# Kernel optimization log

Measured on AMD Instinct MI355X. Metric: run time of the kernel, lower is better.

Reference implementation:

```python
import jax, jax.numpy as jnp
import numpy as np

N_NODES = 50000
N_EDGES = 800000
IN_DIM = 128
HID = 64
OUT_DIM = 128
N_GRAPHS = 128


def setup_inputs() -> dict:
    key = jax.random.key(0)
    ks = jax.random.split(key, 16)

    def lin(k, fan_in, fan_out):
        k1, k2 = jax.random.split(k)
        bound = 1.0 / np.sqrt(fan_in)
        W = jax.random.uniform(k1, (fan_in, fan_out), jnp.float32, -bound, bound)
        b = jax.random.uniform(k2, (fan_out,), jnp.float32, -bound, bound)
        return W, b

    x = jax.random.normal(ks[0], (N_NODES, IN_DIM), jnp.float32)
    edge_index = jax.random.randint(ks[1], (2, N_EDGES), 0, N_NODES, jnp.int64)
    batch = jnp.sort(jax.random.randint(ks[2], (N_NODES,), 0, N_GRAPHS, jnp.int64))

    W_in, b_in = lin(ks[3], IN_DIM, HID)
    W1_0, b1_0 = lin(ks[4], HID, HID)
    W2_0, b2_0 = lin(ks[5], HID, HID)
    W1_1, b1_1 = lin(ks[6], HID, HID)
    W2_1, b2_1 = lin(ks[7], HID, HID)
    W_out, b_out = lin(ks[8], HID, OUT_DIM)

    return dict(x=x, edge_index=edge_index, batch=batch,
                W_in=W_in, b_in=b_in,
                W1_0=W1_0, b1_0=b1_0, W2_0=W2_0, b2_0=b2_0,
                W1_1=W1_1, b1_1=b1_1, W2_1=W2_1, b2_1=b2_1,
                W_out=W_out, b_out=b_out)


def _gin_conv(x, src, dst, W1, b1, W2, b2):
    # aggr[i] = sum_{(s,i) in E} x[s]; GIN (eps=0): h = MLP(x + aggr)
    msgs = x[src]  # [E, HID] gather
    aggr = jax.ops.segment_sum(msgs, dst, num_segments=N_NODES)
    h = x + aggr
    h = jax.nn.relu(h @ W1 + b1)
    return h @ W2 + b2


def reference(x, edge_index, batch,
              W_in, b_in,
              W1_0, b1_0, W2_0, b2_0,
              W1_1, b1_1, W2_1, b2_1,
              W_out, b_out):
    src, dst = edge_index[0], edge_index[1]
    h = x @ W_in + b_in  # proj_in
    # conv 0 (+ReLU; dropout is identity in eval mode)
    h = jax.nn.relu(_gin_conv(h, src, dst, W1_0, b1_0, W2_0, b2_0))
    # conv 1
    h = jax.nn.relu(_gin_conv(h, src, dst, W1_1, b1_1, W2_1, b2_1))
    h = h @ W_out + b_out  # proj_out -> [N, OUT_DIM]
    # global mean pool over graphs
    sums = jax.ops.segment_sum(h, batch, num_segments=N_GRAPHS)
    counts = jax.ops.segment_sum(jnp.ones((h.shape[0],), h.dtype), batch, num_segments=N_GRAPHS)
    graph_emb = sums / jnp.maximum(counts, 1.0)[:, None]  # [N_GRAPHS, OUT_DIM]
    return graph_emb
```

## Files before the change

### kernel.cpp

```cpp
#include <hip/hip_runtime.h>
#include <hip/hip_fp16.h>

#define N_NODES   50000
#define N_EDGES   800000
#define IN_DIM    128
#define HID       64
#define OUT_DIM   128
#define N_GRAPHS  128

#define NBKT      196
#define BBLK      392
#define BSTRIDE   5120
#define CAP       40

#define OFF_GCUR   0
#define OFF_GSUM   196
#define OFF_GSTART 8388
#define OFF_ROWPTR 8518
#define OFF_SRCL   58520
#define OFF_EPAIRS 458520
#define OFF_HA     1462040
#define OFF_HB     2262040

typedef float v2f __attribute__((ext_vector_type(2)));

__device__ __forceinline__ void acc_fp8x8(float acc[8], const uint2 w) {
    const v2f a = __builtin_amdgcn_cvt_pk_f32_fp8(w.x, false);
    const v2f b = __builtin_amdgcn_cvt_pk_f32_fp8(w.x, true);
    const v2f c = __builtin_amdgcn_cvt_pk_f32_fp8(w.y, false);
    const v2f d = __builtin_amdgcn_cvt_pk_f32_fp8(w.y, true);
    acc[0] += a.x; acc[1] += a.y; acc[2] += b.x; acc[3] += b.y;
    acc[4] += c.x; acc[5] += c.y; acc[6] += d.x; acc[7] += d.y;
}

__device__ __forceinline__ uint2 pack_fp8x8(const float f[8]) {
    int w0 = 0, w1 = 0;
    w0 = __builtin_amdgcn_cvt_pk_fp8_f32(f[0], f[1], w0, false);
    w0 = __builtin_amdgcn_cvt_pk_fp8_f32(f[2], f[3], w0, true);
    w1 = __builtin_amdgcn_cvt_pk_fp8_f32(f[4], f[5], w1, false);
    w1 = __builtin_amdgcn_cvt_pk_fp8_f32(f[6], f[7], w1, true);
    uint2 r; r.x = (unsigned)w0; r.y = (unsigned)w1;
    return r;
}

#define BG_SMEM_BYTES 32144

__device__ __forceinline__ void role_bucket(char* smem, const int* __restrict__ ei,
                                            int* __restrict__ gcur,
                                            unsigned int* __restrict__ epairs,
                                            int bid) {
    int* lcnt = (int*)smem;
    unsigned int* stage = (unsigned int*)(smem + NBKT * 4);
    const int t = threadIdx.x;
    for (int i = t; i < NBKT; i += 256) lcnt[i] = 0;
    __syncthreads();
    for (int e0 = bid * 512; e0 < N_EDGES; e0 += BBLK * 512) {
#pragma unroll
        for (int half = 0; half < 2; ++half) {
            const int e = e0 + half * 256 + t;
            if (e < N_EDGES) {
                const unsigned int src = (unsigned int)ei[e];
                const unsigned int dst = (unsigned int)ei[N_EDGES + e];
                const int b = dst >> 8;
                const unsigned int pk = src | (dst << 16);
                const int pos = atomicAdd(&lcnt[b], 1);
                if (pos < CAP) stage[b * CAP + pos] = pk;
                else {
                    const int gp = atomicAdd(&gcur[b], 1);
                    epairs[b * BSTRIDE + gp] = pk;
                }
            }
        }
        __syncthreads();
        if (t < NBKT) {
            int n = lcnt[t]; if (n > CAP) n = CAP;
            if (n >= 16) {
                const int f = n & ~15;
                const int base = atomicAdd(&gcur[t], f);
                if ((base & 3) == 0) {
                    for (int i = 0; i < f; i += 4)
                        *(uint4*)&epairs[t * BSTRIDE + base + i] =
                            *(const uint4*)&stage[t * CAP + i];
                } else {
                    for (int i = 0; i < f; ++i)
                        epairs[t * BSTRIDE + base + i] = stage[t * CAP + i];
                }
                for (int i = 0; i < n - f; ++i)
                    stage[t * CAP + i] = stage[t * CAP + f + i];
                lcnt[t] = n - f;
            } else {
                lcnt[t] = n;
            }
        }
        __syncthreads();
    }
    if (t < NBKT) {
        const int n = lcnt[t];
        if (n > 0) {
            const int base = atomicAdd(&gcur[t], n);
            for (int i = 0; i < n; ++i)
                epairs[t * BSTRIDE + base + i] = stage[t * CAP + i];
        }
    }
}

__device__ __forceinline__ void role_gbound(const int* __restrict__ batch,
                                            int* __restrict__ gstart, int bid) {
    const int n = bid * 256 + threadIdx.x;
    if (n >= N_NODES) return;
    const int b = batch[n];
    if (n == 0) {
        for (int g = 0; g <= b; ++g) gstart[g] = 0;
    } else {
        const int p = batch[n - 1];
        for (int g = p + 1; g <= b; ++g) gstart[g] = n;
    }
    if (n == N_NODES - 1) {
        for (int g = b + 1; g <= N_GRAPHS; ++g) gstart[g] = N_NODES;
    }
}

__global__ __launch_bounds__(256) void k_bg(
        const int* __restrict__ ei, const int* __restrict__ batch,
        int* __restrict__ gcur, unsigned int* __restrict__ epairs,
        int* __restrict__ gstart) {
    __shared__ __attribute__((aligned(16))) char smem[BG_SMEM_BYTES];
    const int bid = blockIdx.x;
    if (bid < BBLK) role_bucket(smem, ei, gcur, epairs, bid);
    else            role_gbound(batch, gstart, bid - BBLK);
}

#define S_X2 132
#define CP_SMEM_BYTES 33280

__device__ __forceinline__ void role_csr(char* smem, const int* __restrict__ gcur,
                                         const unsigned int* __restrict__ epairs,
                                         int* __restrict__ rowptr,
                                         unsigned short* __restrict__ srclist, int b) {
    int* lhist = (int*)smem;
    int* lcur  = lhist + 256;
    int* pws   = lcur + 256;
    int* wtot  = pws + 4;
    int* lsrc  = wtot + 4;
    const int t = threadIdx.x;
    const int lane = t & 63, wv = t >> 6;

    int po = 0;
    for (int j = t; j < b; j += 256) po += gcur[j];
#pragma unroll
    for (int m = 32; m; m >>= 1) po += __shfl_xor(po, m, 64);
    if (lane == 0) pws[wv] = po;
    lhist[t] = 0;
    __syncthreads();
    const int base = pws[0] + pws[1] + pws[2] + pws[3];
    const int cnt = gcur[b];

    for (int i = t; i < cnt; i += 256)
        atomicAdd(&lhist[(epairs[b * BSTRIDE + i] >> 16) & 255], 1);
    __syncthreads();

    const int d = lhist[t];
    int incl = d;
#pragma unroll
    for (int off = 1; off < 64; off <<= 1) {
        const int u = __shfl_up(incl, off, 64);
        if (lane >= off) incl += u;
    }
    if (lane == 63) wtot[wv] = incl;
    __syncthreads();
    int woff = 0;
#pragma unroll
    for (int i = 0; i < 4; ++i) woff += (i < wv) ? wtot[i] : 0;
    const int excl = woff + incl - d;
    lcur[t] = excl;
    const int node = b * 256 + t;
    if (node < N_NODES) rowptr[node] = base + excl;
    if (b == NBKT - 1 && t == 0) rowptr[N_NODES] = base + cnt;
    __syncthreads();

    for (int i = t; i < cnt; i += 256) {
        const unsigned int u = epairs[b * BSTRIDE + i];
        const int pos = atomicAdd(&lcur[(u >> 16) & 255], 1);
        lsrc[pos] = (int)(u & 0xFFFFu);
    }
    __syncthreads();
    for (int i = t; i < cnt; i += 256)
        srclist[base + i] = (unsigned short)lsrc[i];
}

__device__ __forceinline__ void role_proj(char* smem, const float* __restrict__ x,
                                          const float* __restrict__ W,
                                          const float* __restrict__ b,
                                          unsigned char* __restrict__ h8, int bid) {
    __half* A = (__half*)smem;
    float* Wl = (float*)(smem + 64 * S_X2 * 2);
    const int t = threadIdx.x;
    const int nb = bid * 64;
    for (int i = t; i < 64 * HID; i += 256) Wl[i] = W[i];
    for (int i = t; i < 64 * (IN_DIM / 4); i += 256) {
        const int n = i >> 5;
        const int k4 = (i & 31) * 4;
        float4 val = make_float4(0.f, 0.f, 0.f, 0.f);
        if (nb + n < N_NODES)
            val = *(const float4*)(x + (size_t)(nb + n) * IN_DIM + k4);
        union { uint2 u; __half2 h[2]; } pk;
        pk.h[0] = __floats2half2_rn(val.x, val.y);
        pk.h[1] = __floats2half2_rn(val.z, val.w);
        *(uint2*)&A[n * S_X2 + k4] = pk.u;
    }
    __syncthreads();

    const int ln = t & 31;
    const int c0 = (t >> 5) * 8;
    float acc[2][8];
#pragma unroll
    for (int j = 0; j < 2; ++j)
#pragma unroll
        for (int c = 0; c < 8; ++c) acc[j][c] = b[c0 + c];
    for (int k = 0; k < 64; ++k) {
        const float a0 = __half2float(A[ln * S_X2 + k]);
        const float a1 = __half2float(A[(ln + 32) * S_X2 + k]);
        const float4 wA = *(const float4*)&Wl[k * HID + c0];
        const float4 wB = *(const float4*)&Wl[k * HID + c0 + 4];
        const float w[8] = {wA.x, wA.y, wA.z, wA.w, wB.x, wB.y, wB.z, wB.w};
#pragma unroll
        for (int c = 0; c < 8; ++c) {
            acc[0][c] = fmaf(a0, w[c], acc[0][c]);
            acc[1][c] = fmaf(a1, w[c], acc[1][c]);
        }
    }
    __syncthreads();
    for (int i = t; i < 64 * HID; i += 256) Wl[i] = W[64 * HID + i];
    __syncthreads();
    for (int k = 64; k < 128; ++k) {
        const float a0 = __half2float(A[ln * S_X2 + k]);
        const float a1 = __half2float(A[(ln + 32) * S_X2 + k]);
        const float4 wA = *(const float4*)&Wl[(k - 64) * HID + c0];
        const float4 wB = *(const float4*)&Wl[(k - 64) * HID + c0 + 4];
        const float w[8] = {wA.x, wA.y, wA.z, wA.w, wB.x, wB.y, wB.z, wB.w};
#pragma unroll
        for (int c = 0; c < 8; ++c) {
            acc[0][c] = fmaf(a0, w[c], acc[0][c]);
            acc[1][c] = fmaf(a1, w[c], acc[1][c]);
        }
    }
#pragma unroll
    for (int j = 0; j < 2; ++j) {
        const int n = nb + ln + 32 * j;
        if (n < N_NODES) {
            const uint2 p = pack_fp8x8(acc[j]);
            *(uint2*)(h8 + (size_t)n * HID + c0) = p;
        }
    }
}

__global__ __launch_bounds__(256) void k_cp(
        const int* __restrict__ gcur, const unsigned int* __restrict__ epairs,
        const float* __restrict__ x, const float* __restrict__ W,
        const float* __restrict__ b,
        int* __restrict__ rowptr, unsigned short* __restrict__ srcl,
        unsigned char* __restrict__ h8) {
    __shared__ __attribute__((aligned(16))) char smem[CP_SMEM_BYTES];
    const int bid = blockIdx.x;
    if (bid < NBKT) role_csr(smem, gcur, epairs, rowptr, srcl, bid);
    else            role_proj(smem, x, W, b, h8, bid - NBKT);
}

#define S_A 65
template<int POOL>
__global__ __launch_bounds__(256, 4) void k_conv_t(
        const unsigned char* __restrict__ hin8,
        const int* __restrict__ rowptr, const unsigned short* __restrict__ srclist,
        const float* __restrict__ W1, const float* __restrict__ b1,
        const float* __restrict__ W2, const float* __restrict__ b2,
        unsigned char* __restrict__ hout8,
        const int* __restrict__ batch, float* __restrict__ gsum) {
    __shared__ float A[64 * S_A];
    __shared__ float Wl[HID * HID];
    const int t = threadIdx.x;
    for (int i = t; i < HID * HID; i += 256) Wl[i] = W1[i];

    const int nb = blockIdx.x * 64;
    const int grp = t >> 3;
    const int q = t & 7;
#pragma unroll
    for (int pass = 0; pass < 2; ++pass) {
        const int nloc = pass * 32 + grp;
        const int node = nb + nloc;
        float acc[8] = {0.f, 0.f, 0.f, 0.f, 0.f, 0.f, 0.f, 0.f};
        if (node < N_NODES) {
            acc_fp8x8(acc, *(const uint2*)(hin8 + (size_t)node * HID + q * 8));
            const int beg = rowptr[node];
            const int end = rowptr[node + 1];
            int e = beg;
            for (; e + 8 <= end; e += 8) {
                int s[8];
#pragma unroll
                for (int i = 0; i < 8; ++i) s[i] = srclist[e + i];
                uint2 r[8];
#pragma unroll
                for (int i = 0; i < 8; ++i)
                    r[i] = *(const uint2*)(hin8 + (size_t)s[i] * HID + q * 8);
#pragma unroll
                for (int i = 0; i < 8; ++i) acc_fp8x8(acc, r[i]);
            }
            for (; e < end; ++e)
                acc_fp8x8(acc, *(const uint2*)(hin8 + (size_t)srclist[e] * HID + q * 8));
        }
        float* dst = &A[nloc * S_A + q * 8];
#pragma unroll
        for (int i = 0; i < 8; ++i) dst[i] = acc[i];
    }
    __syncthreads();

    const int ln = t & 31;
    const int c0 = (t >> 5) * 8;
    float bb[8];
#pragma unroll
    for (int c = 0; c < 8; ++c) bb[c] = b1[c0 + c];

    float acc2[2][8];
#pragma unroll
    for (int j = 0; j < 2; ++j)
#pragma unroll
        for (int c = 0; c < 8; ++c) acc2[j][c] = bb[c];
    for (int k = 0; k < HID; ++k) {
        const float a0 = A[ln * S_A + k];
        const float a1 = A[(ln + 32) * S_A + k];
        const float4 wA = *(const float4*)&Wl[k * HID + c0];
        const float4 wB = *(const float4*)&Wl[k * HID + c0 + 4];
        const float w[8] = {wA.x, wA.y, wA.z, wA.w, wB.x, wB.y, wB.z, wB.w};
#pragma unroll
        for (int c = 0; c < 8; ++c) {
            acc2[0][c] = fmaf(a0, w[c], acc2[0][c]);
            acc2[1][c] = fmaf(a1, w[c], acc2[1][c]);
        }
    }
    __syncthreads();
#pragma unroll
    for (int j = 0; j < 2; ++j) {
        float* dst = &A[(ln + 32 * j) * S_A + c0];
#pragma unroll
        for (int c = 0; c < 8; ++c) dst[c] = fmaxf(acc2[j][c], 0.0f);
    }
    for (int i = t; i < HID * HID; i += 256) Wl[i] = W2[i];
#pragma unroll
    for (int c = 0; c < 8; ++c) bb[c] = b2[c0 + c];
    __syncthreads();

#pragma unroll
    for (int j = 0; j < 2; ++j)
#pragma unroll
        for (int c = 0; c < 8; ++c) acc2[j][c] = bb[c];
    for (int k = 0; k < HID; ++k) {
        const float a0 = A[ln * S_A + k];
        const float a1 = A[(ln + 32) * S_A + k];
        const float4 wA = *(const float4*)&Wl[k * HID + c0];
        const float4 wB = *(const float4*)&Wl[k * HID + c0 + 4];
        const float w[8] = {wA.x, wA.y, wA.z, wA.w, wB.x, wB.y, wB.z, wB.w};
#pragma unroll
        for (int c = 0; c < 8; ++c) {
            acc2[0][c] = fmaf(a0, w[c], acc2[0][c]);
            acc2[1][c] = fmaf(a1, w[c], acc2[1][c]);
        }
    }
    if constexpr (POOL) {
        const int nlast = (nb + 64 <= N_NODES) ? nb + 63 : N_NODES - 1;
        const int g0 = batch[nb];
        const int g1 = batch[nlast];
        int myg[2];
#pragma unroll
        for (int j = 0; j < 2; ++j) {
            const int n = nb + ln + 32 * j;
            myg[j] = (n < N_NODES) ? batch[n] : -1;
        }
        for (int g = g0; g <= g1; ++g) {
#pragma unroll
            for (int j = 0; j < 2; ++j) {
#pragma unroll
                for (int c = 0; c < 8; ++c) {
                    float v = (myg[j] == g) ? fmaxf(acc2[j][c], 0.0f) : 0.0f;
#pragma unroll
                    for (int m = 16; m; m >>= 1) v += __shfl_xor(v, m, 64);
                    if (ln == 0) atomicAdd(&gsum[g * HID + c0 + c], v);
                }
            }
        }
    } else {
#pragma unroll
        for (int j = 0; j < 2; ++j) {
            const int n = nb + ln + 32 * j;
            if (n < N_NODES) {
                float f[8];
#pragma unroll
                for (int c = 0; c < 8; ++c) f[c] = fmaxf(acc2[j][c], 0.0f);
                const uint2 p = pack_fp8x8(f);
                *(uint2*)(hout8 + (size_t)n * HID + c0) = p;
            }
        }
    }
}

__global__ __launch_bounds__(128) void k_out(
        const float* __restrict__ gsum, const int* __restrict__ gstart,
        const float* __restrict__ Wo, const float* __restrict__ bo,
        float* __restrict__ out) {
    __shared__ float mean[HID];
    const int g = blockIdx.x;
    const int t = threadIdx.x;
    const int cnt = gstart[g + 1] - gstart[g];
    if (t < HID)
        mean[t] = (cnt > 0) ? gsum[g * HID + t] / (float)cnt : 0.0f;
    __syncthreads();
    float o = 0.0f;
    for (int k = 0; k < HID; ++k)
        o = fmaf(mean[k], Wo[k * OUT_DIM + t], o);
    out[g * OUT_DIM + t] = (cnt > 0) ? o + bo[t] : 0.0f;
}

extern "C" void kernel_launch(void* const* d_in, const int* in_sizes, int n_in,
                              void* d_out, int out_size, void* d_ws, size_t ws_size,
                              hipStream_t stream) {
    const float* x     = (const float*)d_in[0];
    const int*   ei    = (const int*)d_in[1];
    const int*   batch = (const int*)d_in[2];
    const float* W_in  = (const float*)d_in[3];
    const float* b_in  = (const float*)d_in[4];
    const float* W1_0  = (const float*)d_in[5];
    const float* b1_0  = (const float*)d_in[6];
    const float* W2_0  = (const float*)d_in[7];
    const float* b2_0  = (const float*)d_in[8];
    const float* W1_1  = (const float*)d_in[9];
    const float* b1_1  = (const float*)d_in[10];
    const float* W2_1  = (const float*)d_in[11];
    const float* b2_1  = (const float*)d_in[12];
    const float* W_out = (const float*)d_in[13];
    const float* b_out = (const float*)d_in[14];
    float* out = (float*)d_out;

    unsigned int*   wsw    = (unsigned int*)d_ws;
    int*            gcur   = (int*)(wsw + OFF_GCUR);
    float*          gsum   = (float*)(wsw + OFF_GSUM);
    int*            gstart = (int*)(wsw + OFF_GSTART);
    int*            rowptr = (int*)(wsw + OFF_ROWPTR);
    unsigned short* srcl   = (unsigned short*)(wsw + OFF_SRCL);
    unsigned int*   epairs = (unsigned int*)(wsw + OFF_EPAIRS);
    unsigned char*  hA     = (unsigned char*)(wsw + OFF_HA);
    unsigned char*  hB     = (unsigned char*)(wsw + OFF_HB);

    const int pi_blocks = (N_NODES + 63) / 64;
    const int cv_blocks = (N_NODES + 63) / 64;
    const int bg_blocks = BBLK + NBKT;
    const int cp_blocks = NBKT + pi_blocks;

    hipMemsetAsync(gcur, 0, (NBKT + N_GRAPHS * HID) * sizeof(int), stream);
    k_bg<<<bg_blocks, 256, 0, stream>>>(ei, batch, gcur, epairs, gstart);
    k_cp<<<cp_blocks, 256, 0, stream>>>(gcur, epairs, x, W_in, b_in,
                                        rowptr, srcl, hA);
    k_conv_t<0><<<cv_blocks, 256, 0, stream>>>(hA, rowptr, srcl,
                                               W1_0, b1_0, W2_0, b2_0, hB,
                                               batch, gsum);
    k_conv_t<1><<<cv_blocks, 256, 0, stream>>>(hB, rowptr, srcl,
                                               W1_1, b1_1, W2_1, b2_1, hA,
                                               batch, gsum);
    k_out<<<N_GRAPHS, 128, 0, stream>>>(gsum, gstart, W_out, b_out, out);
}
```

Baseline: 204.8 us.

## Use bf16 MFMA for input projection and GIN MLP layers

Replaces the scalar FP32 FMA loops in the input projection and both GIN MLPs with bf16 MFMA 16x16x32 instructions. One extra block in the bucketing kernel converts the weights once into transposed, padded bf16 copies in workspace. The per-node aggregates and activations are now staged as bf16 in shared memory, and results pass through a float buffer in shared memory before fp8 packing or pooling. This is meant to cut the ALU-bound matmul time, at the cost of lower intermediate precision and extra shared-memory round trips.

```diff
diff --git a/kernel.cpp b/kernel.cpp
--- a/kernel.cpp
+++ b/kernel.cpp
@@ -21,8 +21,19 @@
 #define OFF_EPAIRS 458520
 #define OFF_HA     1462040
 #define OFF_HB     2262040
+#define OFF_WT     3062040
 
 typedef float v2f __attribute__((ext_vector_type(2)));
+typedef float f32x4 __attribute__((ext_vector_type(4)));
+typedef short bf16x8 __attribute__((ext_vector_type(8)));
+
+union FragU { uint4 u; bf16x8 v; };
+
+__device__ __forceinline__ unsigned short f2bf(float f) {
+    union { float f; unsigned int u; } v; v.f = f;
+    const unsigned int r = v.u + 0x7FFFu + ((v.u >> 16) & 1u);
+    return (unsigned short)(r >> 16);
+}
 
 __device__ __forceinline__ void acc_fp8x8(float acc[8], const uint2 w) {
     const v2f a = __builtin_amdgcn_cvt_pk_f32_fp8(w.x, false);
@@ -120,18 +131,44 @@
     }
 }
 
+__device__ __forceinline__ void role_wprep(const float* __restrict__ Wi,
+                                           const float* __restrict__ W10,
+                                           const float* __restrict__ W20,
+                                           const float* __restrict__ W11,
+                                           const float* __restrict__ W21,
+                                           unsigned short* __restrict__ wtg) {
+    const int t = threadIdx.x;
+    for (int i = t; i < 128 * 64; i += 256) {
+        const int k = i >> 6, c = i & 63;
+        wtg[c * 136 + k] = f2bf(Wi[i]);
+    }
+    const float* Ws[4] = {W10, W20, W11, W21};
+#pragma unroll
+    for (int m = 0; m < 4; ++m) {
+        unsigned short* o = wtg + 8704 + m * 4608;
+        const float* w = Ws[m];
+        for (int i = t; i < 64 * 64; i += 256) {
+            const int k = i >> 6, c = i & 63;
+            o[c * 72 + k] = f2bf(w[i]);
+        }
+    }
+}
+
 __global__ __launch_bounds__(256) void k_bg(
         const int* __restrict__ ei, const int* __restrict__ batch,
         int* __restrict__ gcur, unsigned int* __restrict__ epairs,
-        int* __restrict__ gstart) {
+        int* __restrict__ gstart,
+        const float* __restrict__ Wi, const float* __restrict__ W10,
+        const float* __restrict__ W20, const float* __restrict__ W11,
+        const float* __restrict__ W21, unsigned short* __restrict__ wtg) {
     __shared__ __attribute__((aligned(16))) char smem[BG_SMEM_BYTES];
     const int bid = blockIdx.x;
-    if (bid < BBLK) role_bucket(smem, ei, gcur, epairs, bid);
-    else            role_gbound(batch, gstart, bid - BBLK);
-}
-
-#define S_X2 132
-#define CP_SMEM_BYTES 33280
+    if (bid < BBLK)              role_bucket(smem, ei, gcur, epairs, bid);
+    else if (bid < BBLK + NBKT)  role_gbound(batch, gstart, bid - BBLK);
+    else                         role_wprep(Wi, W10, W20, W11, W21, wtg);
+}
+
+#define CP_SMEM_BYTES 34816
 
 __device__ __forceinline__ void role_csr(char* smem, const int* __restrict__ gcur,
                                          const unsigned int* __restrict__ epairs,
@@ -189,66 +226,70 @@
 }
 
 __device__ __forceinline__ void role_proj(char* smem, const float* __restrict__ x,
-                                          const float* __restrict__ W,
+                                          const unsigned short* __restrict__ Wt_g,
                                           const float* __restrict__ b,
                                           unsigned char* __restrict__ h8, int bid) {
-    __half* A = (__half*)smem;
-    float* Wl = (float*)(smem + 64 * S_X2 * 2);
+    unsigned short* X16 = (unsigned short*)smem;
+    unsigned short* Wt  = (unsigned short*)(smem + 17408);
+    float* OUT32 = (float*)smem;
     const int t = threadIdx.x;
     const int nb = bid * 64;
-    for (int i = t; i < 64 * HID; i += 256) Wl[i] = W[i];
+    {
+        const uint4* s = (const uint4*)Wt_g;
+        uint4* d = (uint4*)Wt;
+        for (int i = t; i < 1088; i += 256) d[i] = s[i];
+    }
     for (int i = t; i < 64 * (IN_DIM / 4); i += 256) {
         const int n = i >> 5;
         const int k4 = (i & 31) * 4;
         float4 val = make_float4(0.f, 0.f, 0.f, 0.f);
         if (nb + n < N_NODES)
             val = *(const float4*)(x + (size_t)(nb + n) * IN_DIM + k4);
-        union { uint2 u; __half2 h[2]; } pk;
-        pk.h[0] = __floats2half2_rn(val.x, val.y);
-        pk.h[1] = __floats2half2_rn(val.z, val.w);
-        *(uint2*)&A[n * S_X2 + k4] = pk.u;
-    }
-    __syncthreads();
-
+        union { uint2 u; unsigned short s[4]; } pk;
+        pk.s[0] = f2bf(val.x); pk.s[1] = f2bf(val.y);
+        pk.s[2] = f2bf(val.z); pk.s[3] = f2bf(val.w);
+        *(uint2*)&X16[n * 136 + k4] = pk.u;
+    }
+    __syncthreads();
+
+    const int l = t & 63;
+    const int m0 = (t >> 6) * 16;
+    const int lrow = l & 15;
+    const int lk = (l >> 4) * 8;
+    FragU a[4];
+#pragma unroll
+    for (int s = 0; s < 4; ++s)
+        a[s].u = *(const uint4*)&X16[(m0 + lrow) * 136 + s * 32 + lk];
+    f32x4 acc[4];
+#pragma unroll
+    for (int n = 0; n < 4; ++n) {
+        const float bv = b[n * 16 + lrow];
+        acc[n] = (f32x4){bv, bv, bv, bv};
+#pragma unroll
+        for (int s = 0; s < 4; ++s) {
+            FragU w;
+            w.u = *(const uint4*)&Wt[(n * 16 + lrow) * 136 + s * 32 + lk];
+            acc[n] = __builtin_amdgcn_mfma_f32_16x16x32_bf16(a[s].v, w.v, acc[n], 0, 0, 0);
+        }
+    }
+    __syncthreads();
+#pragma unroll
+    for (int n = 0; n < 4; ++n)
+#pragma unroll
+        for (int r = 0; r < 4; ++r)
+            OUT32[(m0 + (l >> 4) * 4 + r) * 68 + n * 16 + lrow] = acc[n][r];
+    __syncthreads();
     const int ln = t & 31;
     const int c0 = (t >> 5) * 8;
-    float acc[2][8];
-#pragma unroll
-    for (int j = 0; j < 2; ++j)
-#pragma unroll
-        for (int c = 0; c < 8; ++c) acc[j][c] = b[c0 + c];
-    for (int k = 0; k < 64; ++k) {
-        const float a0 = __half2float(A[ln * S_X2 + k]);
-        const float a1 = __half2float(A[(ln + 32) * S_X2 + k]);
-        const float4 wA = *(const float4*)&Wl[k * HID + c0];
-        const float4 wB = *(const float4*)&Wl[k * HID + c0 + 4];
-        const float w[8] = {wA.x, wA.y, wA.z, wA.w, wB.x, wB.y, wB.z, wB.w};
-#pragma unroll
-        for (int c = 0; c < 8; ++c) {
-            acc[0][c] = fmaf(a0, w[c], acc[0][c]);
-            acc[1][c] = fmaf(a1, w[c], acc[1][c]);
-        }
-    }
-    __syncthreads();
-    for (int i = t; i < 64 * HID; i += 256) Wl[i] = W[64 * HID + i];
-    __syncthreads();
-    for (int k = 64; k < 128; ++k) {
-        const float a0 = __half2float(A[ln * S_X2 + k]);
-        const float a1 = __half2float(A[(ln + 32) * S_X2 + k]);
-        const float4 wA = *(const float4*)&Wl[(k - 64) * HID + c0];
-        const float4 wB = *(const float4*)&Wl[(k - 64) * HID + c0 + 4];
-        const float w[8] = {wA.x, wA.y, wA.z, wA.w, wB.x, wB.y, wB.z, wB.w};
-#pragma unroll
-        for (int c = 0; c < 8; ++c) {
-            acc[0][c] = fmaf(a0, w[c], acc[0][c]);
-            acc[1][c] = fmaf(a1, w[c], acc[1][c]);
-        }
-    }
 #pragma unroll
     for (int j = 0; j < 2; ++j) {
         const int n = nb + ln + 32 * j;
         if (n < N_NODES) {
-            const uint2 p = pack_fp8x8(acc[j]);
+            float f[8];
+            const float* src = &OUT32[(ln + 32 * j) * 68 + c0];
+            *(float4*)&f[0] = *(const float4*)&src[0];
+            *(float4*)&f[4] = *(const float4*)&src[4];
+            const uint2 p = pack_fp8x8(f);
             *(uint2*)(h8 + (size_t)n * HID + c0) = p;
         }
     }
@@ -256,29 +297,39 @@
 
 __global__ __launch_bounds__(256) void k_cp(
         const int* __restrict__ gcur, const unsigned int* __restrict__ epairs,
-        const float* __restrict__ x, const float* __restrict__ W,
+        const float* __restrict__ x, const unsigned short* __restrict__ Wt_g,
         const float* __restrict__ b,
         int* __restrict__ rowptr, unsigned short* __restrict__ srcl,
         unsigned char* __restrict__ h8) {
     __shared__ __attribute__((aligned(16))) char smem[CP_SMEM_BYTES];
     const int bid = blockIdx.x;
     if (bid < NBKT) role_csr(smem, gcur, epairs, rowptr, srcl, bid);
-    else            role_proj(smem, x, W, b, h8, bid - NBKT);
-}
-
-#define S_A 65
+    else            role_proj(smem, x, Wt_g, b, h8, bid - NBKT);
+}
+
+#define S_AB 72
 template<int POOL>
 __global__ __launch_bounds__(256, 4) void k_conv_t(
         const unsigned char* __restrict__ hin8,
         const int* __restrict__ rowptr, const unsigned short* __restrict__ srclist,
-        const float* __restrict__ W1, const float* __restrict__ b1,
-        const float* __restrict__ W2, const float* __restrict__ b2,
+        const unsigned short* __restrict__ W1t_g, const float* __restrict__ b1,
+        const unsigned short* __restrict__ W2t_g, const float* __restrict__ b2,
         unsigned char* __restrict__ hout8,
         const int* __restrict__ batch, float* __restrict__ gsum) {
-    __shared__ float A[64 * S_A];
-    __shared__ float Wl[HID * HID];
+    __shared__ __attribute__((aligned(16))) char csm[36864];
+    unsigned short* A16 = (unsigned short*)csm;
+    unsigned short* H16 = (unsigned short*)(csm + 9216);
+    unsigned short* W1t = (unsigned short*)(csm + 18432);
+    unsigned short* W2t = (unsigned short*)(csm + 27648);
+    float* OUT32 = (float*)csm;
     const int t = threadIdx.x;
-    for (int i = t; i < HID * HID; i += 256) Wl[i] = W1[i];
+    {
+        const uint4* s1 = (const uint4*)W1t_g;
+        const uint4* s2 = (const uint4*)W2t_g;
+        uint4* d1 = (uint4*)W1t;
+        uint4* d2 = (uint4*)W2t;
+        for (int i = t; i < 576; i += 256) { d1[i] = s1[i]; d2[i] = s2[i]; }
+    }
 
     const int nb = blockIdx.x * 64;
     const int grp = t >> 3;
@@ -307,79 +358,86 @@
             for (; e < end; ++e)
                 acc_fp8x8(acc, *(const uint2*)(hin8 + (size_t)srclist[e] * HID + q * 8));
         }
-        float* dst = &A[nloc * S_A + q * 8];
-#pragma unroll
-        for (int i = 0; i < 8; ++i) dst[i] = acc[i];
-    }
+        union { uint4 u; unsigned short s[8]; } ou;
+#pragma unroll
+        for (int c = 0; c < 8; ++c) ou.s[c] = f2bf(acc[c]);
+        *(uint4*)&A16[nloc * S_AB + q * 8] = ou.u;
+    }
+    __syncthreads();
+
+    const int l = t & 63;
+    const int m0 = (t >> 6) * 16;
+    const int lrow = l & 15;
+    const int lk = (l >> 4) * 8;
+
+    FragU a0, a1;
+    a0.u = *(const uint4*)&A16[(m0 + lrow) * S_AB + lk];
+    a1.u = *(const uint4*)&A16[(m0 + lrow) * S_AB + 32 + lk];
+    f32x4 acc1[4];
+#pragma unroll
+    for (int n = 0; n < 4; ++n) {
+        const float bv = b1[n * 16 + lrow];
+        acc1[n] = (f32x4){bv, bv, bv, bv};
+        FragU w0, w1;
+        w0.u = *(const uint4*)&W1t[(n * 16 + lrow) * S_AB + lk];
+        w1.u = *(const uint4*)&W1t[(n * 16 + lrow) * S_AB + 32 + lk];
+        acc1[n] = __builtin_amdgcn_mfma_f32_16x16x32_bf16(a0.v, w0.v, acc1[n], 0, 0, 0);
+        acc1[n] = __builtin_amdgcn_mfma_f32_16x16x32_bf16(a1.v, w1.v, acc1[n], 0, 0, 0);
+    }
+    __syncthreads();
+#pragma unroll
+    for (int n = 0; n < 4; ++n)
+#pragma unroll
+        for (int r = 0; r < 4; ++r) {
+            const int row = m0 + (l >> 4) * 4 + r;
+            H16[row * S_AB + n * 16 + lrow] = f2bf(fmaxf(acc1[n][r], 0.0f));
+        }
+    __syncthreads();
+
+    FragU h0, h1;
+    h0.u = *(const uint4*)&H16[(m0 + lrow) * S_AB + lk];
+    h1.u = *(const uint4*)&H16[(m0 + lrow) * S_AB + 32 + lk];
+    f32x4 acc2[4];
+#pragma unroll
+    for (int n = 0; n < 4; ++n) {
+        const float bv = b2[n * 16 + lrow];
+        acc2[n] = (f32x4){bv, bv, bv, bv};
+        FragU w0, w1;
+        w0.u = *(const uint4*)&W2t[(n * 16 + lrow) * S_AB + lk];
+        w1.u = *(const uint4*)&W2t[(n * 16 + lrow) * S_AB + 32 + lk];
+        acc2[n] = __builtin_amdgcn_mfma_f32_16x16x32_bf16(h0.v, w0.v, acc2[n], 0, 0, 0);
+        acc2[n] = __builtin_amdgcn_mfma_f32_16x16x32_bf16(h1.v, w1.v, acc2[n], 0, 0, 0);
+    }
+    __syncthreads();
+#pragma unroll
+    for (int n = 0; n < 4; ++n)
+#pragma unroll
+        for (int r = 0; r < 4; ++r)
+            OUT32[(m0 + (l >> 4) * 4 + r) * 68 + n * 16 + lrow] = fmaxf(acc2[n][r], 0.0f);
     __syncthreads();
 
     const int ln = t & 31;
     const int c0 = (t >> 5) * 8;
-    float bb[8];
-#pragma unroll
-    for (int c = 0; c < 8; ++c) bb[c] = b1[c0 + c];
-
-    float acc2[2][8];
-#pragma unroll
-    for (int j = 0; j < 2; ++j)
-#pragma unroll
-        for (int c = 0; c < 8; ++c) acc2[j][c] = bb[c];
-    for (int k = 0; k < HID; ++k) {
-        const float a0 = A[ln * S_A + k];
-        const float a1 = A[(ln + 32) * S_A + k];
-        const float4 wA = *(const float4*)&Wl[k * HID + c0];
-        const float4 wB = *(const float4*)&Wl[k * HID + c0 + 4];
-        const float w[8] = {wA.x, wA.y, wA.z, wA.w, wB.x, wB.y, wB.z, wB.w};
-#pragma unroll
-        for (int c = 0; c < 8; ++c) {
-            acc2[0][c] = fmaf(a0, w[c], acc2[0][c]);
-            acc2[1][c] = fmaf(a1, w[c], acc2[1][c]);
-        }
-    }
-    __syncthreads();
-#pragma unroll
-    for (int j = 0; j < 2; ++j) {
-        float* dst = &A[(ln + 32 * j) * S_A + c0];
-#pragma unroll
-        for (int c = 0; c < 8; ++c) dst[c] = fmaxf(acc2[j][c], 0.0f);
-    }
-    for (int i = t; i < HID * HID; i += 256) Wl[i] = W2[i];
-#pragma unroll
-    for (int c = 0; c < 8; ++c) bb[c] = b2[c0 + c];
-    __syncthreads();
-
-#pragma unroll
-    for (int j = 0; j < 2; ++j)
-#pragma unroll
-        for (int c = 0; c < 8; ++c) acc2[j][c] = bb[c];
-    for (int k = 0; k < HID; ++k) {
-        const float a0 = A[ln * S_A + k];
-        const float a1 = A[(ln + 32) * S_A + k];
-        const float4 wA = *(const float4*)&Wl[k * HID + c0];
-        const float4 wB = *(const float4*)&Wl[k * HID + c0 + 4];
-        const float w[8] = {wA.x, wA.y, wA.z, wA.w, wB.x, wB.y, wB.z, wB.w};
-#pragma unroll
-        for (int c = 0; c < 8; ++c) {
-            acc2[0][c] = fmaf(a0, w[c], acc2[0][c]);
-            acc2[1][c] = fmaf(a1, w[c], acc2[1][c]);
-        }
-    }
     if constexpr (POOL) {
         const int nlast = (nb + 64 <= N_NODES) ? nb + 63 : N_NODES - 1;
         const int g0 = batch[nb];
         const int g1 = batch[nlast];
         int myg[2];
+        float f[2][8];
 #pragma unroll
         for (int j = 0; j < 2; ++j) {
             const int n = nb + ln + 32 * j;
             myg[j] = (n < N_NODES) ? batch[n] : -1;
+            const float* src = &OUT32[(ln + 32 * j) * 68 + c0];
+            *(float4*)&f[j][0] = *(const float4*)&src[0];
+            *(float4*)&f[j][4] = *(const float4*)&src[4];
         }
         for (int g = g0; g <= g1; ++g) {
 #pragma unroll
             for (int j = 0; j < 2; ++j) {
 #pragma unroll
                 for (int c = 0; c < 8; ++c) {
-                    float v = (myg[j] == g) ? fmaxf(acc2[j][c], 0.0f) : 0.0f;
+                    float v = (myg[j] == g) ? f[j][c] : 0.0f;
 #pragma unroll
                     for (int m = 16; m; m >>= 1) v += __shfl_xor(v, m, 64);
                     if (ln == 0) atomicAdd(&gsum[g * HID + c0 + c], v);
@@ -392,8 +450,9 @@
             const int n = nb + ln + 32 * j;
             if (n < N_NODES) {
                 float f[8];
-#pragma unroll
-                for (int c = 0; c < 8; ++c) f[c] = fmaxf(acc2[j][c], 0.0f);
+                const float* src = &OUT32[(ln + 32 * j) * 68 + c0];
+                *(float4*)&f[0] = *(const float4*)&src[0];
+                *(float4*)&f[4] = *(const float4*)&src[4];
                 const uint2 p = pack_fp8x8(f);
                 *(uint2*)(hout8 + (size_t)n * HID + c0) = p;
             }
@@ -447,21 +506,29 @@
     unsigned int*   epairs = (unsigned int*)(wsw + OFF_EPAIRS);
     unsigned char*  hA     = (unsigned char*)(wsw + OFF_HA);
     unsigned char*  hB     = (unsigned char*)(wsw + OFF_HB);
+    unsigned short* wtg    = (unsigned short*)(wsw + OFF_WT);
+
+    unsigned short* wt_in = wtg;
+    unsigned short* wt10  = wtg + 8704;
+    unsigned short* wt20  = wtg + 13312;
+    unsigned short* wt11  = wtg + 17920;
+    unsigned short* wt21  = wtg + 22528;
 
     const int pi_blocks = (N_NODES + 63) / 64;
     const int cv_blocks = (N_NODES + 63) / 64;
-    const int bg_blocks = BBLK + NBKT;
+    const int bg_blocks = BBLK + NBKT + 1;
     const int cp_blocks = NBKT + pi_blocks;
 
     hipMemsetAsync(gcur, 0, (NBKT + N_GRAPHS * HID) * sizeof(int), stream);
-    k_bg<<<bg_blocks, 256, 0, stream>>>(ei, batch, gcur, epairs, gstart);
-    k_cp<<<cp_blocks, 256, 0, stream>>>(gcur, epairs, x, W_in, b_in,
+    k_bg<<<bg_blocks, 256, 0, stream>>>(ei, batch, gcur, epairs, gstart,
+                                        W_in, W1_0, W2_0, W1_1, W2_1, wtg);
+    k_cp<<<cp_blocks, 256, 0, stream>>>(gcur, epairs, x, wt_in, b_in,
                                         rowptr, srcl, hA);
     k_conv_t<0><<<cv_blocks, 256, 0, stream>>>(hA, rowptr, srcl,
-                                               W1_0, b1_0, W2_0, b2_0, hB,
+                                               wt10, b1_0, wt20, b2_0, hB,
                                                batch, gsum);
     k_conv_t<1><<<cv_blocks, 256, 0, stream>>>(hB, rowptr, srcl,
-                                               W1_1, b1_1, W2_1, b2_1, hA,
+                                               wt11, b1_1, wt21, b2_1, hA,
                                                batch, gsum);
     k_out<<<N_GRAPHS, 128, 0, stream>>>(gsum, gstart, W_out, b_out, out);
 }
```

New measurement: 187.2 us. 8.6% less time.
